# Kernel optimization log

Hardware: AMD Instinct MI355X
Metric: run time of the kernel (lower is better)

## Reference

```python
import jax, jax.numpy as jnp
import numpy as np

N = 100000      # nodes
E = 1600000     # edges (no self-loops; self-loops added in reference, per PyG defaults)
IN = 128        # in_size
HID = 32        # hide_size (per-head channels)
HEADS = 4       # n_heads
OUT = 128       # out_size
NEG_SLOPE = 0.2 # PyG GATConv default negative_slope


def setup_inputs() -> dict:
    key = jax.random.key(0)
    ks = jax.random.split(key, 8)
    x = jax.random.normal(ks[0], (N, IN), jnp.float32)
    # edges guaranteed non-self-loop: dst = (src + offset) % N with offset in [1, N)
    src = jax.random.randint(ks[1], (E,), 0, N, dtype=jnp.int32)
    off = jax.random.randint(ks[2], (E,), 1, N, dtype=jnp.int32)
    dst = ((src + off) % N).astype(jnp.int32)
    edge_index = jnp.stack([src, dst])  # [2, E]
    edge_weight = jax.random.uniform(ks[3], (E,), jnp.float32)
    glorot = lambda k, shape, fan: jax.random.normal(k, shape, jnp.float32) / np.sqrt(fan).astype(np.float32)
    W_gat = glorot(ks[4], (IN, HEADS * HID), IN)      # GATConv lin weight (bias=False)
    att_src = glorot(ks[5], (HEADS, HID), HID)        # GATConv att_src
    att_dst = glorot(ks[6], (HEADS, HID), HID)        # GATConv att_dst
    W_gcn = glorot(ks[7], (HEADS * HID, OUT), HEADS * HID)  # GCNConv weight (bias=False)
    return {"x": x, "edge_index": edge_index, "edge_weight": edge_weight,
            "W_gat": W_gat, "att_src": att_src, "att_dst": att_dst, "W_gcn": W_gcn}


def reference(x, edge_index, edge_weight, W_gat, att_src, att_dst, W_gcn):
    n = x.shape[0]
    loop = jnp.arange(n, dtype=edge_index.dtype)
    src = jnp.concatenate([edge_index[0], loop])  # add self-loops (PyG default)
    dst = jnp.concatenate([edge_index[1], loop])

    # ---- GATConv (concat heads, bias=False) ----
    xp = (x @ W_gat).reshape(n, HEADS, HID)                  # [N,H,C]
    a_s = jnp.einsum('nhc,hc->nh', xp, att_src)              # [N,H]
    a_d = jnp.einsum('nhc,hc->nh', xp, att_dst)
    alpha = jax.nn.leaky_relu(a_s[src] + a_d[dst], NEG_SLOPE)  # [E+N,H]
    m = jax.ops.segment_max(alpha, dst, num_segments=n)     # segment softmax over incoming edges
    e = jnp.exp(alpha - m[dst])
    denom = jax.ops.segment_sum(e, dst, num_segments=n)
    a = e / denom[dst]                                       # [E+N,H]
    y_gat = jax.ops.segment_sum(xp[src] * a[:, :, None], dst, num_segments=n)
    y_gat = y_gat.reshape(n, HEADS * HID)                    # [N, H*C]

    # ---- GCNConv (normalize=True, bias=False), self-loop weight = 1 ----
    ew = jnp.concatenate([edge_weight, jnp.ones((n,), edge_weight.dtype)])
    deg = jax.ops.segment_sum(ew, dst, num_segments=n)
    dinv = jnp.where(deg > 0, jax.lax.rsqrt(deg), 0.0)
    norm = dinv[src] * ew * dinv[dst]                        # [E+N]
    h = y_gat @ W_gcn                                        # [N, OUT]
    out = jax.ops.segment_sum(h[src] * norm[:, None], dst, num_segments=n)
    return out
```

## Files before the change

### kernel.cpp

```cpp
#include <hip/hip_runtime.h>

#define NN 100000
#define EE 1600000
#define TOT (EE + NN)
#define NEG 0.2f
#define NB 256
#define CH 391
#define TILE 4096
#define NTILES ((EE + TILE - 1) / TILE)
#define GEMM_BLKS ((NN + 63) / 64)

typedef unsigned int uint;
typedef unsigned short ushort;

__device__ inline ushort f2bf(float f) {
    uint u = __float_as_uint(f);
    return (ushort)((u + 0x7fff + ((u >> 16) & 1)) >> 16);
}

__device__ inline int imin(int a, int b) { return a < b ? a : b; }


__launch_bounds__(256) __global__
void k_bcount(const int* __restrict__ dst, int* __restrict__ bcnt) {
    __shared__ int h[NB];
    int t = threadIdx.x;
    h[t] = 0;
    __syncthreads();
    int base = blockIdx.x * TILE;
#pragma unroll
    for (int r = 0; r < 16; ++r) {
        int e = base + r * 256 + t;
        if (e < EE) atomicAdd(&h[dst[e] / CH], 1);
    }
    __syncthreads();
    if (h[t]) atomicAdd(&bcnt[t], h[t]);
}


__launch_bounds__(NB) __global__
void k_bprefix(const int* __restrict__ bcnt, int* __restrict__ boff,
               int* __restrict__ bcsr, int* __restrict__ bfill) {
    __shared__ int s1[NB], s2[NB];
    int t = threadIdx.x;
    int c = bcnt[t];
    int nb0 = t * CH;
    int nib = imin(nb0 + CH, NN) - nb0;
    s1[t] = c; s2[t] = c + nib;
    __syncthreads();
    for (int off = 1; off < NB; off <<= 1) {
        int a = (t >= off) ? s1[t - off] : 0;
        int b = (t >= off) ? s2[t - off] : 0;
        __syncthreads();
        s1[t] += a; s2[t] += b;
        __syncthreads();
    }
    int ex = s1[t] - c;
    boff[t] = ex;
    bfill[t] = ex;
    bcsr[t] = s2[t] - (c + nib);
    if (t == NB - 1) boff[NB] = EE;
}


__launch_bounds__(256) __global__
void k_bin(const int* __restrict__ src, const int* __restrict__ dst,
           const float* __restrict__ ew, int* __restrict__ bfill,
           long long* __restrict__ binned) {
    __shared__ long long recs[TILE];
    __shared__ ushort    bkt[TILE];
    __shared__ int hist[NB], eoff[NB], gbase[NB];
    int t = threadIdx.x;
    hist[t] = 0;
    __syncthreads();
    int base = blockIdx.x * TILE;
    int cnt = imin(TILE, EE - base);
    long long rec[16]; int binfo[16];
#pragma unroll
    for (int r = 0; r < 16; ++r) {
        int i = r * 256 + t;
        if (i < cnt) {
            int e = base + i;
            int s = src[e], d = dst[e];
            float w = ew[e];
            int b = d / CH;
            int ldst = d - b * CH;
            int rk = atomicAdd(&hist[b], 1);
            rec[r] = (long long)(uint)(s | (ldst << 17)) |
                     ((long long)__float_as_uint(w) << 32);
            binfo[r] = b | (rk << 8);
        }
    }
    __syncthreads();
    int c = hist[t];
    eoff[t] = c;
    __syncthreads();
    for (int off = 1; off < NB; off <<= 1) {
        int a = (t >= off) ? eoff[t - off] : 0;
        __syncthreads();
        eoff[t] += a;
        __syncthreads();
    }
    int ex = eoff[t] - c;
    gbase[t] = atomicAdd(&bfill[t], c);
    eoff[t] = ex;
    __syncthreads();
#pragma unroll
    for (int r = 0; r < 16; ++r) {
        int i = r * 256 + t;
        if (i < cnt) {
            int b = binfo[r] & 255, rk = binfo[r] >> 8;
            int slot = eoff[b] + rk;
            recs[slot] = rec[r];
            bkt[slot] = (ushort)b;
        }
    }
    __syncthreads();
#pragma unroll
    for (int r = 0; r < 16; ++r) {
        int i = r * 256 + t;
        if (i < cnt) {
            int b = bkt[i];
            binned[gbase[b] + (i - eoff[b])] = recs[i];
        }
    }
}


__device__ __forceinline__ void gemm1_body(
    int bid, const float* __restrict__ A, const float* __restrict__ W,
    ushort* __restrict__ C16, const float* __restrict__ att_s,
    const float* __restrict__ att_d, float* __restrict__ a_s,
    float* __restrict__ a_d) {
    int lane = threadIdx.x & 63;
    int cg = __builtin_amdgcn_readfirstlane(threadIdx.x >> 6);
    int row = bid * 64 + lane;
    bool valid = row < NN;
    if (!valid) row = NN - 1;
    const float* __restrict__ a = A + (size_t)row * 128;
    const float* __restrict__ w = W + cg * 32;
    float acc[32];
#pragma unroll
    for (int c = 0; c < 32; ++c) acc[c] = 0.f;
    float4 xv = *(const float4*)(a);
    for (int k = 0; k < 128; k += 4) {
        float4 nx = xv;
        if (k < 124) nx = *(const float4*)(a + k + 4);
        float xs[4] = {xv.x, xv.y, xv.z, xv.w};
#pragma unroll
        for (int kk = 0; kk < 4; ++kk) {
            const float* wr = w + (k + kk) * 128;
            float xk = xs[kk];
#pragma unroll
            for (int c = 0; c < 32; ++c) acc[c] = fmaf(xk, wr[c], acc[c]);
        }
        xv = nx;
    }
    if (valid) {
        ushort* o = C16 + (size_t)row * 128 + cg * 32;
#pragma unroll
        for (int c = 0; c < 32; c += 8) {
            uint4 p;
            p.x = (uint)f2bf(acc[c+0]) | ((uint)f2bf(acc[c+1]) << 16);
            p.y = (uint)f2bf(acc[c+2]) | ((uint)f2bf(acc[c+3]) << 16);
            p.z = (uint)f2bf(acc[c+4]) | ((uint)f2bf(acc[c+5]) << 16);
            p.w = (uint)f2bf(acc[c+6]) | ((uint)f2bf(acc[c+7]) << 16);
            *(uint4*)(o + c) = p;
        }
        const float* as = att_s + cg * 32;
        const float* ad = att_d + cg * 32;
        float s0 = 0.f, s1 = 0.f;
#pragma unroll
        for (int c = 0; c < 32; ++c) {
            s0 = fmaf(acc[c], as[c], s0);
            s1 = fmaf(acc[c], ad[c], s1);
        }
        a_s[row * 4 + cg] = s0;
        a_d[row * 4 + cg] = s1;
    }
}


__launch_bounds__(256) __global__
void k_fine_gemm(const long long* __restrict__ binned, const int* __restrict__ boff,
                 const int* __restrict__ bcsr, int* __restrict__ row_off,
                 long long* __restrict__ csr,
                 const float* __restrict__ A, const float* __restrict__ W,
                 ushort* __restrict__ C16, const float* __restrict__ att_s,
                 const float* __restrict__ att_d, float* __restrict__ a_s,
                 float* __restrict__ a_d) {
    if (blockIdx.x >= NB) {
        gemm1_body(blockIdx.x - NB, A, W, C16, att_s, att_d, a_s, a_d);
        return;
    }
    __shared__ int hist[CH];
    __shared__ int excl[CH];
    __shared__ int sc[512];
    int t = threadIdx.x;
    int b = blockIdx.x;
    int e0 = boff[b], e1 = boff[b + 1];
    int nb0 = b * CH;
    int nnode = imin(CH, NN - nb0);
    const int2* __restrict__ bn = (const int2*)binned;
    hist[t] = 0;
    if (t + 256 < CH) hist[t + 256] = 0;
    __syncthreads();
    for (int i = e0 + t; i < e1; i += 256)
        atomicAdd(&hist[bn[i].x >> 17], 1);
    __syncthreads();
    int v0 = (t < nnode) ? hist[t] + 1 : 0;
    int v1 = (t + 256 < nnode) ? hist[t + 256] + 1 : 0;
    sc[t] = v0; sc[t + 256] = v1;
    __syncthreads();
    for (int off = 1; off < 512; off <<= 1) {
        int a0 = (t >= off) ? sc[t - off] : 0;
        int a1 = (t + 256 >= off) ? sc[t + 256 - off] : 0;
        __syncthreads();
        sc[t] += a0; sc[t + 256] += a1;
        __syncthreads();
    }
    int csr0 = bcsr[b];
    if (t < nnode) {
        excl[t] = csr0 + sc[t] - v0;
        row_off[nb0 + t] = excl[t];
    }
    if (t + 256 < nnode) {
        excl[t + 256] = csr0 + sc[t + 256] - v1;
        row_off[nb0 + t + 256] = excl[t + 256];
    }
    if (b == 0 && t == 0) row_off[NN] = TOT;
    hist[t] = 0;
    if (t + 256 < CH) hist[t + 256] = 0;
    __syncthreads();
    for (int i = e0 + t; i < e1; i += 256) {
        int2 r = bn[i];
        int ld = r.x >> 17;
        int rk = atomicAdd(&hist[ld], 1);
        long long rec = (long long)(uint)(r.x & 0x1FFFF) |
                        ((long long)(uint)r.y << 32);
        csr[excl[ld] + rk] = rec;
    }
    __syncthreads();
    for (int i = t; i < nnode; i += 256) {
        int n = nb0 + i;
        csr[excl[i] + hist[i]] = (long long)(uint)n | (0x3F800000LL << 32);
    }
}


__launch_bounds__(256) __global__
void k_gemm2(const float* __restrict__ A, const float* __restrict__ W,
             ushort* __restrict__ C16, const float* __restrict__ dscale) {
    int lane = threadIdx.x & 63;
    int cg = __builtin_amdgcn_readfirstlane(threadIdx.x >> 6);
    int row = blockIdx.x * 64 + lane;
    bool valid = row < NN;
    if (!valid) row = NN - 1;
    const float* __restrict__ a = A + (size_t)row * 128;
    const float* __restrict__ w = W + cg * 32;
    float acc[32];
#pragma unroll
    for (int c = 0; c < 32; ++c) acc[c] = 0.f;
    float4 xv = *(const float4*)(a);
    for (int k = 0; k < 128; k += 4) {
        float4 nx = xv;
        if (k < 124) nx = *(const float4*)(a + k + 4);
        float xs[4] = {xv.x, xv.y, xv.z, xv.w};
#pragma unroll
        for (int kk = 0; kk < 4; ++kk) {
            const float* wr = w + (k + kk) * 128;
            float xk = xs[kk];
#pragma unroll
            for (int c = 0; c < 32; ++c) acc[c] = fmaf(xk, wr[c], acc[c]);
        }
        xv = nx;
    }
    if (valid) {
        float sc = dscale[row];
        ushort* o = C16 + (size_t)row * 128 + cg * 32;
#pragma unroll
        for (int c = 0; c < 32; c += 8) {
            uint4 p;
            p.x = (uint)f2bf(acc[c+0]*sc) | ((uint)f2bf(acc[c+1]*sc) << 16);
            p.y = (uint)f2bf(acc[c+2]*sc) | ((uint)f2bf(acc[c+3]*sc) << 16);
            p.z = (uint)f2bf(acc[c+4]*sc) | ((uint)f2bf(acc[c+5]*sc) << 16);
            p.w = (uint)f2bf(acc[c+6]*sc) | ((uint)f2bf(acc[c+7]*sc) << 16);
            *(uint4*)(o + c) = p;
        }
    }
}


__launch_bounds__(256) __global__
void k_gat(const int* __restrict__ row_off, const int2* __restrict__ csr,
           const float* __restrict__ a_s, const float* __restrict__ a_d,
           const ushort* __restrict__ xp16,
           float* __restrict__ ygat, float* __restrict__ dinv) {
    int lane = threadIdx.x & 63;
    int node = blockIdx.x * 4 + (threadIdx.x >> 6);
    int base = row_off[node], end = row_off[node + 1];
    int grp = lane >> 4, sl = lane & 15, h2 = sl >> 2;
    float adh = a_d[node * 4 + h2];
    float acc[8];
#pragma unroll
    for (int j = 0; j < 8; ++j) acc[j] = 0.f;
    float den = 0.f, wsum = 0.f;
    int na = end - 1;
    int i0 = base + grp;
    int2 eA = csr[imin(i0, na)];
    int2 eB = csr[imin(i0 + 4, na)];
    for (int i = i0; i < end; i += 8) {
        int2 eA2 = csr[imin(i + 8,  na)];
        int2 eB2 = csr[imin(i + 12, na)];
        uint4 qA = *(const uint4*)(xp16 + (size_t)eA.x * 128 + sl * 8);
        uint4 qB = *(const uint4*)(xp16 + (size_t)eB.x * 128 + sl * 8);
        float alA = a_s[eA.x * 4 + h2] + adh;
        alA = alA > 0.f ? alA : NEG * alA;
        float awA = __expf(alA);
        float awB = 0.f, wB = 0.f;
        if (i + 4 < end) {
            float alB = a_s[eB.x * 4 + h2] + adh;
            alB = alB > 0.f ? alB : NEG * alB;
            awB = __expf(alB);
            wB = __int_as_float(eB.y);
        }
        den  += awA + awB;
        wsum += __int_as_float(eA.y) + wB;
        acc[0] = fmaf(awA, __uint_as_float(qA.x << 16),         fmaf(awB, __uint_as_float(qB.x << 16),         acc[0]));
        acc[1] = fmaf(awA, __uint_as_float(qA.x & 0xffff0000u), fmaf(awB, __uint_as_float(qB.x & 0xffff0000u), acc[1]));
        acc[2] = fmaf(awA, __uint_as_float(qA.y << 16),         fmaf(awB, __uint_as_float(qB.y << 16),         acc[2]));
        acc[3] = fmaf(awA, __uint_as_float(qA.y & 0xffff0000u), fmaf(awB, __uint_as_float(qB.y & 0xffff0000u), acc[3]));
        acc[4] = fmaf(awA, __uint_as_float(qA.z << 16),         fmaf(awB, __uint_as_float(qB.z << 16),         acc[4]));
        acc[5] = fmaf(awA, __uint_as_float(qA.z & 0xffff0000u), fmaf(awB, __uint_as_float(qB.z & 0xffff0000u), acc[5]));
        acc[6] = fmaf(awA, __uint_as_float(qA.w << 16),         fmaf(awB, __uint_as_float(qB.w << 16),         acc[6]));
        acc[7] = fmaf(awA, __uint_as_float(qA.w & 0xffff0000u), fmaf(awB, __uint_as_float(qB.w & 0xffff0000u), acc[7]));
        eA = eA2; eB = eB2;
    }
#pragma unroll
    for (int j = 0; j < 8; ++j) {
        acc[j] += __shfl_xor(acc[j], 16);
        acc[j] += __shfl_xor(acc[j], 32);
    }
    den  += __shfl_xor(den, 16);   den  += __shfl_xor(den, 32);
    wsum += __shfl_xor(wsum, 16);  wsum += __shfl_xor(wsum, 32);
    if (grp == 0) {
        float il = 1.f / den;
        float* o = ygat + (size_t)node * 128 + sl * 8;
        *(float4*)(o)     = make_float4(acc[0]*il, acc[1]*il, acc[2]*il, acc[3]*il);
        *(float4*)(o + 4) = make_float4(acc[4]*il, acc[5]*il, acc[6]*il, acc[7]*il);
        if (sl == 0) dinv[node] = rsqrtf(wsum);
    }
}


__launch_bounds__(256) __global__
void k_gcn(const int* __restrict__ row_off, const int2* __restrict__ csr,
           const float* __restrict__ dinv, const ushort* __restrict__ h16,
           float* __restrict__ out) {
    int lane = threadIdx.x & 63;
    int node = blockIdx.x * 4 + (threadIdx.x >> 6);
    int base = row_off[node], end = row_off[node + 1];
    float dn = dinv[node];
    int grp = lane >> 4, sl = lane & 15;
    float acc[8];
#pragma unroll
    for (int j = 0; j < 8; ++j) acc[j] = 0.f;
    int na = end - 1;
    int i0 = base + grp;
    int2 eA = csr[imin(i0, na)];
    int2 eB = csr[imin(i0 + 4, na)];
    for (int i = i0; i < end; i += 8) {
        int2 eA2 = csr[imin(i + 8,  na)];
        int2 eB2 = csr[imin(i + 12, na)];
        uint4 qA = *(const uint4*)(h16 + (size_t)eA.x * 128 + sl * 8);
        uint4 qB = *(const uint4*)(h16 + (size_t)eB.x * 128 + sl * 8);
        float cA = __int_as_float(eA.y) * dn;
        float cB = (i + 4 < end) ? __int_as_float(eB.y) * dn : 0.f;
        acc[0] = fmaf(cA, __uint_as_float(qA.x << 16),         fmaf(cB, __uint_as_float(qB.x << 16),         acc[0]));
        acc[1] = fmaf(cA, __uint_as_float(qA.x & 0xffff0000u), fmaf(cB, __uint_as_float(qB.x & 0xffff0000u), acc[1]));
        acc[2] = fmaf(cA, __uint_as_float(qA.y << 16),         fmaf(cB, __uint_as_float(qB.y << 16),         acc[2]));
        acc[3] = fmaf(cA, __uint_as_float(qA.y & 0xffff0000u), fmaf(cB, __uint_as_float(qB.y & 0xffff0000u), acc[3]));
        acc[4] = fmaf(cA, __uint_as_float(qA.z << 16),         fmaf(cB, __uint_as_float(qB.z << 16),         acc[4]));
        acc[5] = fmaf(cA, __uint_as_float(qA.z & 0xffff0000u), fmaf(cB, __uint_as_float(qB.z & 0xffff0000u), acc[5]));
        acc[6] = fmaf(cA, __uint_as_float(qA.w << 16),         fmaf(cB, __uint_as_float(qB.w << 16),         acc[6]));
        acc[7] = fmaf(cA, __uint_as_float(qA.w & 0xffff0000u), fmaf(cB, __uint_as_float(qB.w & 0xffff0000u), acc[7]));
        eA = eA2; eB = eB2;
    }
#pragma unroll
    for (int j = 0; j < 8; ++j) {
        acc[j] += __shfl_xor(acc[j], 16);
        acc[j] += __shfl_xor(acc[j], 32);
    }
    if (grp == 0) {
        float* o = out + (size_t)node * 128 + sl * 8;
        *(float4*)(o)     = make_float4(acc[0], acc[1], acc[2], acc[3]);
        *(float4*)(o + 4) = make_float4(acc[4], acc[5], acc[6], acc[7]);
    }
}


extern "C" void kernel_launch(void* const* d_in, const int* in_sizes, int n_in,
                              void* d_out, int out_size, void* d_ws, size_t ws_size,
                              hipStream_t stream) {
    const float* x    = (const float*)d_in[0];
    const int*   ei   = (const int*)  d_in[1];
    const float* ew   = (const float*)d_in[2];
    const float* Wg   = (const float*)d_in[3];
    const float* atts = (const float*)d_in[4];
    const float* attd = (const float*)d_in[5];
    const float* Wc   = (const float*)d_in[6];
    float* out = (float*)d_out;

    float* ygat  = (float*)d_ws;
    float* a_s   = ygat + 12800000;
    float* a_d   = a_s + 400000;
    float* dinvp = a_d + 400000;
    int* row_off = (int*)(dinvp + 100000);
    int* bcnt    = row_off + 100004;
    int* boff    = bcnt + NB;
    int* bcsr    = boff + NB + 1;
    int* bfill   = bcsr + NB;
    long long* csr = (long long*)(bfill + NB + 1);
    ushort* xp16 = (ushort*)(csr + 1700000);
    ushort* h16  = xp16 + 12800000;
    long long* binned = (long long*)h16;

    const int* srcv = ei;
    const int* dstv = ei + EE;

    hipMemsetAsync(bcnt, 0, NB * sizeof(int), stream);
    k_bcount <<<NTILES, 256, 0, stream>>>(dstv, bcnt);
    k_bprefix<<<1, NB, 0, stream>>>(bcnt, boff, bcsr, bfill);
    k_bin    <<<NTILES, 256, 0, stream>>>(srcv, dstv, ew, bfill, binned);
    k_fine_gemm<<<NB + GEMM_BLKS, 256, 0, stream>>>(
        binned, boff, bcsr, row_off, csr,
        x, Wg, xp16, atts, attd, a_s, a_d);
    k_gat  <<<NN / 4, 256, 0, stream>>>(row_off, (const int2*)csr, a_s, a_d, xp16,
                                        ygat, dinvp);
    k_gemm2<<<GEMM_BLKS, 256, 0, stream>>>(ygat, Wc, h16, dinvp);
    k_gcn  <<<NN / 4, 256, 0, stream>>>(row_off, (const int2*)csr, dinvp, h16, out);
}
```

Measured before the change: 486.7 us.

## Fuse GAT aggregation with second GEMM via shared-memory tile

Each block now aggregates GAT outputs for 64 nodes into an LDS tile, then immediately multiplies by W_gcn and writes bf16 h scaled by dinv. This removes the fp32 ygat intermediate written to and read from global memory, and one kernel launch. In exchange, blocks are coarser with large LDS usage, reducing occupancy for the latency-bound gather phase.

```diff
diff --git a/kernel.cpp b/kernel.cpp
--- a/kernel.cpp
+++ b/kernel.cpp
@@ -9,6 +9,7 @@
 #define TILE 4096
 #define NTILES ((EE + TILE - 1) / TILE)
 #define GEMM_BLKS ((NN + 63) / 64)
+#define LDA 132
 
 typedef unsigned int uint;
 typedef unsigned short ushort;
@@ -249,22 +250,95 @@
 
 
 __launch_bounds__(256) __global__
-void k_gemm2(const float* __restrict__ A, const float* __restrict__ W,
-             ushort* __restrict__ C16, const float* __restrict__ dscale) {
+void k_gat_g2(const int* __restrict__ row_off, const int2* __restrict__ csr,
+              const float* __restrict__ a_s, const float* __restrict__ a_d,
+              const ushort* __restrict__ xp16, const float* __restrict__ W,
+              ushort* __restrict__ h16, float* __restrict__ dinv) {
+    __shared__ float As[64 * LDA];
+    __shared__ float sdinv[64];
     int lane = threadIdx.x & 63;
-    int cg = __builtin_amdgcn_readfirstlane(threadIdx.x >> 6);
-    int row = blockIdx.x * 64 + lane;
+    int wv = threadIdx.x >> 6;
+    int grp = lane >> 4, sl = lane & 15, h2 = sl >> 2;
+    int nbase = blockIdx.x * 64;
+
+    for (int rnd = 0; rnd < 16; ++rnd) {
+        int r = (rnd << 2) | wv;
+        int node = nbase + r;
+        if (node < NN) {
+            int base = row_off[node], end = row_off[node + 1];
+            float adh = a_d[node * 4 + h2];
+            float acc[8];
+#pragma unroll
+            for (int j = 0; j < 8; ++j) acc[j] = 0.f;
+            float den = 0.f, wsum = 0.f;
+            int na = end - 1;
+            int i0 = base + grp;
+            int2 eA = csr[imin(i0, na)];
+            int2 eB = csr[imin(i0 + 4, na)];
+            for (int i = i0; i < end; i += 8) {
+                int2 eA2 = csr[imin(i + 8,  na)];
+                int2 eB2 = csr[imin(i + 12, na)];
+                uint4 qA = *(const uint4*)(xp16 + (size_t)eA.x * 128 + sl * 8);
+                uint4 qB = *(const uint4*)(xp16 + (size_t)eB.x * 128 + sl * 8);
+                float alA = a_s[eA.x * 4 + h2] + adh;
+                alA = alA > 0.f ? alA : NEG * alA;
+                float awA = __expf(alA);
+                float awB = 0.f, wB = 0.f;
+                if (i + 4 < end) {
+                    float alB = a_s[eB.x * 4 + h2] + adh;
+                    alB = alB > 0.f ? alB : NEG * alB;
+                    awB = __expf(alB);
+                    wB = __int_as_float(eB.y);
+                }
+                den  += awA + awB;
+                wsum += __int_as_float(eA.y) + wB;
+                acc[0] = fmaf(awA, __uint_as_float(qA.x << 16),         fmaf(awB, __uint_as_float(qB.x << 16),         acc[0]));
+                acc[1] = fmaf(awA, __uint_as_float(qA.x & 0xffff0000u), fmaf(awB, __uint_as_float(qB.x & 0xffff0000u), acc[1]));
+                acc[2] = fmaf(awA, __uint_as_float(qA.y << 16),         fmaf(awB, __uint_as_float(qB.y << 16),         acc[2]));
+                acc[3] = fmaf(awA, __uint_as_float(qA.y & 0xffff0000u), fmaf(awB, __uint_as_float(qB.y & 0xffff0000u), acc[3]));
+                acc[4] = fmaf(awA, __uint_as_float(qA.z << 16),         fmaf(awB, __uint_as_float(qB.z << 16),         acc[4]));
+                acc[5] = fmaf(awA, __uint_as_float(qA.z & 0xffff0000u), fmaf(awB, __uint_as_float(qB.z & 0xffff0000u), acc[5]));
+                acc[6] = fmaf(awA, __uint_as_float(qA.w << 16),         fmaf(awB, __uint_as_float(qB.w << 16),         acc[6]));
+                acc[7] = fmaf(awA, __uint_as_float(qA.w & 0xffff0000u), fmaf(awB, __uint_as_float(qB.w & 0xffff0000u), acc[7]));
+                eA = eA2; eB = eB2;
+            }
+#pragma unroll
+            for (int j = 0; j < 8; ++j) {
+                acc[j] += __shfl_xor(acc[j], 16);
+                acc[j] += __shfl_xor(acc[j], 32);
+            }
+            den  += __shfl_xor(den, 16);   den  += __shfl_xor(den, 32);
+            wsum += __shfl_xor(wsum, 16);  wsum += __shfl_xor(wsum, 32);
+            if (grp == 0) {
+                float il = 1.f / den;
+                float* o = &As[r * LDA + sl * 8];
+                *(float4*)(o)     = make_float4(acc[0]*il, acc[1]*il, acc[2]*il, acc[3]*il);
+                *(float4*)(o + 4) = make_float4(acc[4]*il, acc[5]*il, acc[6]*il, acc[7]*il);
+                if (sl == 0) {
+                    float dv = rsqrtf(wsum);
+                    sdinv[r] = dv;
+                    dinv[node] = dv;
+                }
+            }
+        } else if (grp == 0) {
+            float* o = &As[r * LDA + sl * 8];
+            *(float4*)(o)     = make_float4(0.f, 0.f, 0.f, 0.f);
+            *(float4*)(o + 4) = make_float4(0.f, 0.f, 0.f, 0.f);
+            if (sl == 0) sdinv[r] = 0.f;
+        }
+    }
+    __syncthreads();
+
+    int cg = __builtin_amdgcn_readfirstlane(wv);
+    int row = nbase + lane;
     bool valid = row < NN;
-    if (!valid) row = NN - 1;
-    const float* __restrict__ a = A + (size_t)row * 128;
     const float* __restrict__ w = W + cg * 32;
+    const float* __restrict__ a = &As[lane * LDA];
     float acc[32];
 #pragma unroll
     for (int c = 0; c < 32; ++c) acc[c] = 0.f;
-    float4 xv = *(const float4*)(a);
     for (int k = 0; k < 128; k += 4) {
-        float4 nx = xv;
-        if (k < 124) nx = *(const float4*)(a + k + 4);
+        float4 xv = *(const float4*)(a + k);
         float xs[4] = {xv.x, xv.y, xv.z, xv.w};
 #pragma unroll
         for (int kk = 0; kk < 4; ++kk) {
@@ -273,11 +347,10 @@
 #pragma unroll
             for (int c = 0; c < 32; ++c) acc[c] = fmaf(xk, wr[c], acc[c]);
         }
-        xv = nx;
     }
     if (valid) {
-        float sc = dscale[row];
-        ushort* o = C16 + (size_t)row * 128 + cg * 32;
+        float sc = sdinv[lane];
+        ushort* o = h16 + (size_t)row * 128 + cg * 32;
 #pragma unroll
         for (int c = 0; c < 32; c += 8) {
             uint4 p;
@@ -287,68 +360,6 @@
             p.w = (uint)f2bf(acc[c+6]*sc) | ((uint)f2bf(acc[c+7]*sc) << 16);
             *(uint4*)(o + c) = p;
         }
-    }
-}
-
-
-__launch_bounds__(256) __global__
-void k_gat(const int* __restrict__ row_off, const int2* __restrict__ csr,
-           const float* __restrict__ a_s, const float* __restrict__ a_d,
-           const ushort* __restrict__ xp16,
-           float* __restrict__ ygat, float* __restrict__ dinv) {
-    int lane = threadIdx.x & 63;
-    int node = blockIdx.x * 4 + (threadIdx.x >> 6);
-    int base = row_off[node], end = row_off[node + 1];
-    int grp = lane >> 4, sl = lane & 15, h2 = sl >> 2;
-    float adh = a_d[node * 4 + h2];
-    float acc[8];
-#pragma unroll
-    for (int j = 0; j < 8; ++j) acc[j] = 0.f;
-    float den = 0.f, wsum = 0.f;
-    int na = end - 1;
-    int i0 = base + grp;
-    int2 eA = csr[imin(i0, na)];
-    int2 eB = csr[imin(i0 + 4, na)];
-    for (int i = i0; i < end; i += 8) {
-        int2 eA2 = csr[imin(i + 8,  na)];
-        int2 eB2 = csr[imin(i + 12, na)];
-        uint4 qA = *(const uint4*)(xp16 + (size_t)eA.x * 128 + sl * 8);
-        uint4 qB = *(const uint4*)(xp16 + (size_t)eB.x * 128 + sl * 8);
-        float alA = a_s[eA.x * 4 + h2] + adh;
-        alA = alA > 0.f ? alA : NEG * alA;
-        float awA = __expf(alA);
-        float awB = 0.f, wB = 0.f;
-        if (i + 4 < end) {
-            float alB = a_s[eB.x * 4 + h2] + adh;
-            alB = alB > 0.f ? alB : NEG * alB;
-            awB = __expf(alB);
-            wB = __int_as_float(eB.y);
-        }
-        den  += awA + awB;
-        wsum += __int_as_float(eA.y) + wB;
-        acc[0] = fmaf(awA, __uint_as_float(qA.x << 16),         fmaf(awB, __uint_as_float(qB.x << 16),         acc[0]));
-        acc[1] = fmaf(awA, __uint_as_float(qA.x & 0xffff0000u), fmaf(awB, __uint_as_float(qB.x & 0xffff0000u), acc[1]));
-        acc[2] = fmaf(awA, __uint_as_float(qA.y << 16),         fmaf(awB, __uint_as_float(qB.y << 16),         acc[2]));
-        acc[3] = fmaf(awA, __uint_as_float(qA.y & 0xffff0000u), fmaf(awB, __uint_as_float(qB.y & 0xffff0000u), acc[3]));
-        acc[4] = fmaf(awA, __uint_as_float(qA.z << 16),         fmaf(awB, __uint_as_float(qB.z << 16),         acc[4]));
-        acc[5] = fmaf(awA, __uint_as_float(qA.z & 0xffff0000u), fmaf(awB, __uint_as_float(qB.z & 0xffff0000u), acc[5]));
-        acc[6] = fmaf(awA, __uint_as_float(qA.w << 16),         fmaf(awB, __uint_as_float(qB.w << 16),         acc[6]));
-        acc[7] = fmaf(awA, __uint_as_float(qA.w & 0xffff0000u), fmaf(awB, __uint_as_float(qB.w & 0xffff0000u), acc[7]));
-        eA = eA2; eB = eB2;
-    }
-#pragma unroll
-    for (int j = 0; j < 8; ++j) {
-        acc[j] += __shfl_xor(acc[j], 16);
-        acc[j] += __shfl_xor(acc[j], 32);
-    }
-    den  += __shfl_xor(den, 16);   den  += __shfl_xor(den, 32);
-    wsum += __shfl_xor(wsum, 16);  wsum += __shfl_xor(wsum, 32);
-    if (grp == 0) {
-        float il = 1.f / den;
-        float* o = ygat + (size_t)node * 128 + sl * 8;
-        *(float4*)(o)     = make_float4(acc[0]*il, acc[1]*il, acc[2]*il, acc[3]*il);
-        *(float4*)(o + 4) = make_float4(acc[4]*il, acc[5]*il, acc[6]*il, acc[7]*il);
-        if (sl == 0) dinv[node] = rsqrtf(wsum);
     }
 }
 
@@ -411,8 +422,7 @@
     const float* Wc   = (const float*)d_in[6];
     float* out = (float*)d_out;
 
-    float* ygat  = (float*)d_ws;
-    float* a_s   = ygat + 12800000;
+    float* a_s   = (float*)d_ws;
     float* a_d   = a_s + 400000;
     float* dinvp = a_d + 400000;
     int* row_off = (int*)(dinvp + 100000);
@@ -435,8 +445,7 @@
     k_fine_gemm<<<NB + GEMM_BLKS, 256, 0, stream>>>(
         binned, boff, bcsr, row_off, csr,
         x, Wg, xp16, atts, attd, a_s, a_d);
-    k_gat  <<<NN / 4, 256, 0, stream>>>(row_off, (const int2*)csr, a_s, a_d, xp16,
-                                        ygat, dinvp);
-    k_gemm2<<<GEMM_BLKS, 256, 0, stream>>>(ygat, Wc, h16, dinvp);
+    k_gat_g2<<<GEMM_BLKS, 256, 0, stream>>>(row_off, (const int2*)csr, a_s, a_d,
+                                            xp16, Wc, h16, dinvp);
     k_gcn  <<<NN / 4, 256, 0, stream>>>(row_off, (const int2*)csr, dinvp, h16, out);
 }
```

Result: faster. 472.6 us (-2.9%).
